# Kernel tuning notes

Hardware: AMD Instinct MI355X
Metric: run time of the kernel (lower is better)

Reference implementation:

```python
import jax, jax.numpy as jnp
import numpy as np

H = 32  # GRU hidden size


def _conv1d(x, w, b, stride, pad):
    # x: (B, Cin, L), w: (Cout, Cin, K)
    y = jax.lax.conv_general_dilated(
        x, w, window_strides=(stride,), padding=[(pad, pad)],
        dimension_numbers=('NCH', 'OIH', 'NCH'))
    return y + b[None, :, None]


def setup_inputs() -> dict:
    key = jax.random.key(0)
    ks = jax.random.split(key, 16)
    B = 16384
    inp = {
        'past_samples': jax.random.normal(ks[0], (B, 2000), jnp.float32),
        'velocity': jax.random.uniform(ks[1], (B,), jnp.float32),
        'log_pitch': jax.random.normal(ks[2], (B,), jnp.float32),
        'time': jax.random.uniform(ks[3], (B,), jnp.float32),
        'hidden_state': jax.random.normal(ks[4], (B, H), jnp.float32),
        # conv stack params
        'w1': jax.random.normal(ks[5], (4, 1, 31), jnp.float32) * 0.1,
        'b1': jnp.zeros((4,), jnp.float32),
        'w2': jax.random.normal(ks[6], (8, 4, 15), jnp.float32) * 0.1,
        'b2': jnp.zeros((8,), jnp.float32),
        'w3': jax.random.normal(ks[7], (16, 8, 7), jnp.float32) * 0.1,
        'b3': jnp.zeros((16,), jnp.float32),
        # GRU params (torch layout: rows = [r; z; n])
        'w_ih': jax.random.normal(ks[8], (3 * H, 19), jnp.float32) * 0.1,
        'w_hh': jax.random.normal(ks[9], (3 * H, H), jnp.float32) * 0.1,
        'b_ih': jnp.zeros((3 * H,), jnp.float32),
        'b_hh': jnp.zeros((3 * H,), jnp.float32),
        # projection
        'w_proj': jax.random.normal(ks[10], (2, H), jnp.float32) * 0.1,
        'b_proj': jnp.zeros((2,), jnp.float32),
    }
    return inp


def reference(past_samples, velocity, log_pitch, time, hidden_state,
              w1, b1, w2, b2, w3, b3, w_ih, w_hh, b_ih, b_hh, w_proj, b_proj):
    x = past_samples[:, None, :]                       # (B,1,2000)
    x = jax.nn.relu(_conv1d(x, w1, b1, 4, 15))         # (B,4,500)
    x = jax.nn.relu(_conv1d(x, w2, b2, 4, 7))          # (B,8,125)
    x = jax.nn.relu(_conv1d(x, w3, b3, 4, 3))          # (B,16,32)
    ctx = jnp.mean(x, axis=2)                          # adaptive avg pool -> (B,16)

    rnn_in = jnp.concatenate(
        [ctx, velocity[:, None], log_pitch[:, None], time[:, None]], axis=1)  # (B,19)

    # single GRU step (torch GRUCell math)
    gi = rnn_in @ w_ih.T + b_ih                        # (B,3H)
    gh = hidden_state @ w_hh.T + b_hh                  # (B,3H)
    r = jax.nn.sigmoid(gi[:, :H] + gh[:, :H])
    z = jax.nn.sigmoid(gi[:, H:2 * H] + gh[:, H:2 * H])
    n = jnp.tanh(gi[:, 2 * H:] + r * gh[:, 2 * H:])
    new_hidden = (1.0 - z) * n + z * hidden_state      # (B,H)

    out = new_hidden @ w_proj.T + b_proj               # (B,2)
    mu, log_sigma = out[:, :1], out[:, 1:]
    sigma = jnp.exp(log_sigma)
    return (mu, sigma, new_hidden)
```

## Files before the change

kernel.cpp:

```cpp
#include <hip/hip_runtime.h>
#include <hip/hip_fp16.h>
#include <math.h>


typedef _Float16 h2 __attribute__((ext_vector_type(2)));
typedef _Float16 h4 __attribute__((ext_vector_type(4)));
typedef _Float16 h8 __attribute__((ext_vector_type(8)));
typedef float f4 __attribute__((ext_vector_type(4)));

__device__ __forceinline__ float fdot2(h2 a, h2 b, float c)
{
#if defined(__has_builtin)
#if __has_builtin(__builtin_amdgcn_fdot2)
    return __builtin_amdgcn_fdot2(a, b, c, false);
#else
    return c + (float)a.x * (float)b.x + (float)a.y * (float)b.y;
#endif
#else
    return c + (float)a.x * (float)b.x + (float)a.y * (float)b.y;
#endif
}

__device__ __forceinline__ h8 ld_b8(const _Float16* p)
{
    h4 lo = *(const h4*)p;
    h4 hi = *(const h4*)(p + 4);
    return (h8){lo.x, lo.y, lo.z, lo.w, hi.x, hi.y, hi.z, hi.w};
}

__global__ void pack_weights(const float* __restrict__ w1,
                             const float* __restrict__ w2,
                             const float* __restrict__ w3,
                             const float* __restrict__ w_ih,
                             _Float16* __restrict__ hws,
                             float* __restrict__ wihp)
{
    for (int idx = threadIdx.x; idx < 64; idx += 256) {
        int c = idx >> 4, jp = idx & 15;
        int j0 = 2 * jp, j1 = j0 + 1;
        float f0 = (j0 == 0) ? 0.0f : w1[c * 31 + j0 - 1];
        float f1 = w1[c * 31 + j1 - 1];
        hws[2 * idx]     = (_Float16)f0;
        hws[2 * idx + 1] = (_Float16)f1;
    }
    for (int i = threadIdx.x; i < 1024; i += 256) {
        int kk = i >> 9, l = (i >> 3) & 63, j = i & 7;
        int c = l & 15, k = kk * 32 + ((l >> 4) << 3) + j;
        int ci = k >> 4, tap = k & 15;
        float v = (c < 8 && tap < 15) ? w2[(c * 4 + ci) * 15 + tap] : 0.0f;
        hws[1024 + i] = (_Float16)v;
    }
    for (int i = threadIdx.x; i < 1024; i += 256) {
        int kk = i >> 9, l = (i >> 3) & 63, j = i & 7;
        int c = l & 15, k = kk * 32 + ((l >> 4) << 3) + j;
        int ci = k >> 3, tap = k & 7;
        float v = (tap < 7) ? w3[(c * 8 + ci) * 7 + tap] : 0.0f;
        hws[2048 + i] = (_Float16)v;
    }
    for (int idx = threadIdx.x; idx < 96 * 20; idx += 256) {
        int r = idx / 20, c = idx % 20;
        wihp[idx] = (c < 19) ? w_ih[r * 19 + c] : 0.0f;
    }
}

__device__ __forceinline__ void conv1_pos(const _Float16* __restrict__ xh,
                                          _Float16* __restrict__ y1h,
                                          const h2* __restrict__ w1p,
                                          const float* __restrict__ b1,
                                          int p, int h0)
{
    const h4* src = (const h4*)(xh + h0);
    h2 xp[16];
#pragma unroll
    for (int j = 0; j < 8; ++j) {
        h4 v = src[j];
        xp[2 * j]     = (h2){v.x, v.y};
        xp[2 * j + 1] = (h2){v.z, v.w};
    }
    float a0 = b1[0], a1 = b1[1], a2 = b1[2], a3 = b1[3];
#pragma unroll
    for (int j = 0; j < 16; ++j) {
        a0 = fdot2(xp[j], w1p[j],      a0);
        a1 = fdot2(xp[j], w1p[16 + j], a1);
        a2 = fdot2(xp[j], w1p[32 + j], a2);
        a3 = fdot2(xp[j], w1p[48 + j], a3);
    }
    y1h[7 + p]        = (_Float16)fmaxf(a0, 0.0f);
    y1h[512 + 7 + p]  = (_Float16)fmaxf(a1, 0.0f);
    y1h[1024 + 7 + p] = (_Float16)fmaxf(a2, 0.0f);
    y1h[1536 + 7 + p] = (_Float16)fmaxf(a3, 0.0f);
}

__global__ void __launch_bounds__(64, 3)
wavernn_fused(const float* __restrict__ past,
              const float* __restrict__ velocity,
              const float* __restrict__ log_pitch,
              const float* __restrict__ time_in,
              const float* __restrict__ hidden,
              const float* __restrict__ b1,
              const float* __restrict__ b2,
              const float* __restrict__ b3,
              const float* __restrict__ wihp,
              const float* __restrict__ w_hh,
              const float* __restrict__ b_ih, const float* __restrict__ b_hh,
              const float* __restrict__ w_proj, const float* __restrict__ b_proj,
              const _Float16* __restrict__ hws,
              float* __restrict__ out, int B)
{
    __shared__ __align__(16) _Float16 X[1056];
    __shared__ __align__(16) _Float16 y1h[2048];
    __shared__ float rnn[20];
    __shared__ float hs[32];

    _Float16* const xbuf = X;
    _Float16* const y2h  = X;
    float* const gis     = (float*)X;
    float* const ghs     = (float*)X + 96;

    const h2* const w1p = (const h2*)hws;
    const h8* const wf2 = (const h8*)(hws + 1024);
    const h8* const wf3 = (const h8*)(hws + 2048);

    const int t = threadIdx.x;
    const int b = blockIdx.x;

    const float4* row4 = (const float4*)(past + (size_t)b * 2000);

    if (t < 16) { xbuf[t] = (_Float16)0.0f; xbuf[1032 + t] = (_Float16)0.0f; }
    if (t < 48) { int c = t / 12, k = t % 12;
                  y1h[c * 512 + (k < 7 ? k : 500 + k)] = (_Float16)0.0f; }
    if (t < 32) hs[t] = hidden[(size_t)b * 32 + t];
    if (t == 0) rnn[16] = velocity[b];
    if (t == 1) rnn[17] = log_pitch[b];
    if (t == 2) rnn[18] = time_in[b];
    if (t == 3) rnn[19] = 0.0f;

#pragma unroll
    for (int j = 0; j < 4; ++j) {
        int i = t + 64 * j;
        if (i < 254) {
            float4 q = row4[i];
            h4 hv = {(_Float16)q.x, (_Float16)q.y, (_Float16)q.z, (_Float16)q.w};
            *(h4*)(xbuf + 16 + 4 * i) = hv;
        }
    }
    __syncthreads();

#pragma unroll
    for (int j = 0; j < 4; ++j) {
        int p = t + 64 * j;
        if (p < 250) conv1_pos(xbuf, y1h, w1p, b1, p, 4 * p);
    }
    __syncthreads();

#pragma unroll
    for (int j = 0; j < 4; ++j) {
        int i = t + 64 * j;
        if (i < 254) {
            float4 q = row4[246 + i];
            h4 hv = {(_Float16)q.x, (_Float16)q.y, (_Float16)q.z, (_Float16)q.w};
            *(h4*)(xbuf + 16 + 4 * i) = hv;
        }
    }
    __syncthreads();

#pragma unroll
    for (int j = 0; j < 4; ++j) {
        int p = 250 + t + 64 * j;
        if (p < 500) conv1_pos(xbuf, y1h, w1p, b1, p, 4 * p - 984);
    }
    __syncthreads();

    if (t < 56) { int c = t / 7, k = t % 7;
                  y2h[c * 132 + (k < 3 ? k : 125 + k)] = (_Float16)0.0f; }
    {
        const int o = t >> 4, q = t & 15;
        const int ci0 = o >> 1, tp0 = (o & 1) * 8;
        float b2v[4];
#pragma unroll
        for (int r = 0; r < 4; ++r) b2v[r] = b2[(o * 4 + r) & 7];
        const h8 a0 = wf2[t];
        const h8 a1 = wf2[64 + t];
#pragma unroll
        for (int T = 0; T < 8; ++T) {
            const int p = T * 16 + q;
            h8 x0 = ld_b8(y1h + 512 * ci0 + 4 * p + tp0);
            h8 x1 = ld_b8(y1h + 512 * (ci0 + 2) + 4 * p + tp0);
            f4 acc = {0.0f, 0.0f, 0.0f, 0.0f};
            acc = __builtin_amdgcn_mfma_f32_16x16x32_f16(a0, x0, acc, 0, 0, 0);
            acc = __builtin_amdgcn_mfma_f32_16x16x32_f16(a1, x1, acc, 0, 0, 0);
            if (t < 32 && p < 125) {
#pragma unroll
                for (int r = 0; r < 4; ++r)
                    y2h[(o * 4 + r) * 132 + 3 + p] =
                        (_Float16)fmaxf(acc[r] + b2v[r], 0.0f);
            }
        }
    }
    __syncthreads();

    {
        const int o = t >> 4, q = t & 15;
        float b3v[4];
#pragma unroll
        for (int r = 0; r < 4; ++r) b3v[r] = b3[o * 4 + r];
        const h8 a0 = wf3[t];
        const h8 a1 = wf3[64 + t];
        h8 x00 = ld_b8(y2h + 132 * o + 4 * q);
        h8 x01 = ld_b8(y2h + 132 * (4 + o) + 4 * q);
        h8 x10 = ld_b8(y2h + 132 * o + 4 * (16 + q));
        h8 x11 = ld_b8(y2h + 132 * (4 + o) + 4 * (16 + q));
        const f4 z = {0.0f, 0.0f, 0.0f, 0.0f};
        f4 d0 = __builtin_amdgcn_mfma_f32_16x16x32_f16(a0, x00, z, 0, 0, 0);
        d0 = __builtin_amdgcn_mfma_f32_16x16x32_f16(a1, x01, d0, 0, 0, 0);
        f4 d1 = __builtin_amdgcn_mfma_f32_16x16x32_f16(a0, x10, z, 0, 0, 0);
        d1 = __builtin_amdgcn_mfma_f32_16x16x32_f16(a1, x11, d1, 0, 0, 0);
#pragma unroll
        for (int r = 0; r < 4; ++r) {
            float v = fmaxf(d0[r] + b3v[r], 0.0f) + fmaxf(d1[r] + b3v[r], 0.0f);
            v += __shfl_xor(v, 1); v += __shfl_xor(v, 2);
            v += __shfl_xor(v, 4); v += __shfl_xor(v, 8);
            if (q == 0) rnn[o * 4 + r] = v * (1.0f / 32.0f);
        }
    }
    __syncthreads();

    {
        float rv[20];
#pragma unroll
        for (int j = 0; j < 20; ++j) rv[j] = rnn[j];

        float a = b_ih[t];
        const float4* wr = (const float4*)(wihp + t * 20);
#pragma unroll
        for (int j = 0; j < 5; ++j) {
            float4 q = wr[j];
            a += rv[4 * j] * q.x + rv[4 * j + 1] * q.y +
                 rv[4 * j + 2] * q.z + rv[4 * j + 3] * q.w;
        }
        gis[t] = a;
        if (t < 32) {
            float a2 = b_ih[64 + t];
            const float4* wr2 = (const float4*)(wihp + (64 + t) * 20);
#pragma unroll
            for (int j = 0; j < 5; ++j) {
                float4 q = wr2[j];
                a2 += rv[4 * j] * q.x + rv[4 * j + 1] * q.y +
                      rv[4 * j + 2] * q.z + rv[4 * j + 3] * q.w;
            }
            gis[64 + t] = a2;
        }

        float hv[32];
#pragma unroll
        for (int j = 0; j < 32; ++j) hv[j] = hs[j];

        float g = b_hh[t];
        const float4* wh = (const float4*)(w_hh + t * 32);
#pragma unroll
        for (int j = 0; j < 8; ++j) {
            float4 q = wh[j];
            g += hv[4 * j] * q.x + hv[4 * j + 1] * q.y +
                 hv[4 * j + 2] * q.z + hv[4 * j + 3] * q.w;
        }
        ghs[t] = g;
        if (t < 32) {
            float g2 = b_hh[64 + t];
            const float4* wh2 = (const float4*)(w_hh + (64 + t) * 32);
#pragma unroll
            for (int j = 0; j < 8; ++j) {
                float4 q = wh2[j];
                g2 += hv[4 * j] * q.x + hv[4 * j + 1] * q.y +
                      hv[4 * j + 2] * q.z + hv[4 * j + 3] * q.w;
            }
            ghs[64 + t] = g2;
        }
    }
    __syncthreads();

    if (t < 32) {
        const int j = t;
        float r = 1.0f / (1.0f + expf(-(gis[j] + ghs[j])));
        float z = 1.0f / (1.0f + expf(-(gis[32 + j] + ghs[32 + j])));
        float n = tanhf(gis[64 + j] + r * ghs[64 + j]);
        float nh = (1.0f - z) * n + z * hs[j];
        out[(size_t)2 * B + (size_t)b * 32 + j] = nh;

        float p0 = nh * w_proj[j];
        float p1 = nh * w_proj[32 + j];
        p0 += __shfl_xor(p0, 16); p1 += __shfl_xor(p1, 16);
        p0 += __shfl_xor(p0, 8);  p1 += __shfl_xor(p1, 8);
        p0 += __shfl_xor(p0, 4);  p1 += __shfl_xor(p1, 4);
        p0 += __shfl_xor(p0, 2);  p1 += __shfl_xor(p1, 2);
        p0 += __shfl_xor(p0, 1);  p1 += __shfl_xor(p1, 1);
        if (j == 0) {
            out[b] = p0 + b_proj[0];
            out[B + b] = expf(p1 + b_proj[1]);
        }
    }
}

extern "C" void kernel_launch(void* const* d_in, const int* in_sizes, int n_in,
                              void* d_out, int out_size, void* d_ws, size_t ws_size,
                              hipStream_t stream)
{
    const float* past      = (const float*)d_in[0];
    const float* velocity  = (const float*)d_in[1];
    const float* log_pitch = (const float*)d_in[2];
    const float* time_in   = (const float*)d_in[3];
    const float* hidden    = (const float*)d_in[4];
    const float* w1  = (const float*)d_in[5];
    const float* b1  = (const float*)d_in[6];
    const float* w2  = (const float*)d_in[7];
    const float* b2  = (const float*)d_in[8];
    const float* w3  = (const float*)d_in[9];
    const float* b3  = (const float*)d_in[10];
    const float* wih = (const float*)d_in[11];
    const float* whh = (const float*)d_in[12];
    const float* bih = (const float*)d_in[13];
    const float* bhh = (const float*)d_in[14];
    const float* wpr = (const float*)d_in[15];
    const float* bpr = (const float*)d_in[16];

    const int B = in_sizes[0] / 2000;
    _Float16* hws = (_Float16*)d_ws;
    float* wihp = (float*)((char*)d_ws + 8192);

    pack_weights<<<dim3(1), dim3(256), 0, stream>>>(w1, w2, w3, wih, hws, wihp);

    wavernn_fused<<<dim3(B), dim3(64), 0, stream>>>(
        past, velocity, log_pitch, time_in, hidden,
        b1, b2, b3, wihp, whh, bih, bhh, wpr, bpr,
        (const _Float16*)hws, (float*)d_out, B);
}
```

Before: 257.1 us.

## Move conv1 to MFMA and switch activations to position-major channel-interleaved layout

Replaces the per-thread fdot2 conv1 with a 16x16x32 MFMA over im2col-style windows and loads the whole 2000-sample row into shared memory at once instead of two halves. Intermediate activations are stored position-major with channels interleaved, so conv2/conv3 operand loads become single aligned h8 reads, and the weight packing is reordered to match. This removes two syncs and the scalar dot-product loop, at the cost of larger shared buffers. Launch bounds also go from 3 to 4 blocks per CU.

```diff
diff --git a/kernel.cpp b/kernel.cpp
--- a/kernel.cpp
+++ b/kernel.cpp
@@ -7,19 +7,6 @@
 typedef _Float16 h4 __attribute__((ext_vector_type(4)));
 typedef _Float16 h8 __attribute__((ext_vector_type(8)));
 typedef float f4 __attribute__((ext_vector_type(4)));
-
-__device__ __forceinline__ float fdot2(h2 a, h2 b, float c)
-{
-#if defined(__has_builtin)
-#if __has_builtin(__builtin_amdgcn_fdot2)
-    return __builtin_amdgcn_fdot2(a, b, c, false);
-#else
-    return c + (float)a.x * (float)b.x + (float)a.y * (float)b.y;
-#endif
-#else
-    return c + (float)a.x * (float)b.x + (float)a.y * (float)b.y;
-#endif
-}
 
 __device__ __forceinline__ h8 ld_b8(const _Float16* p)
 {
@@ -35,27 +22,25 @@
                              _Float16* __restrict__ hws,
                              float* __restrict__ wihp)
 {
-    for (int idx = threadIdx.x; idx < 64; idx += 256) {
-        int c = idx >> 4, jp = idx & 15;
-        int j0 = 2 * jp, j1 = j0 + 1;
-        float f0 = (j0 == 0) ? 0.0f : w1[c * 31 + j0 - 1];
-        float f1 = w1[c * 31 + j1 - 1];
-        hws[2 * idx]     = (_Float16)f0;
-        hws[2 * idx + 1] = (_Float16)f1;
+    for (int i = threadIdx.x; i < 512; i += 256) {
+        int l = i >> 3, j = i & 7;
+        int c = l & 15, k = ((l >> 4) << 3) + j;
+        float v = (c < 4 && k >= 1) ? w1[c * 31 + (k - 1)] : 0.0f;
+        hws[i] = (_Float16)v;
     }
     for (int i = threadIdx.x; i < 1024; i += 256) {
         int kk = i >> 9, l = (i >> 3) & 63, j = i & 7;
         int c = l & 15, k = kk * 32 + ((l >> 4) << 3) + j;
-        int ci = k >> 4, tap = k & 15;
+        int tap = k >> 2, ci = k & 3;
         float v = (c < 8 && tap < 15) ? w2[(c * 4 + ci) * 15 + tap] : 0.0f;
-        hws[1024 + i] = (_Float16)v;
+        hws[512 + i] = (_Float16)v;
     }
     for (int i = threadIdx.x; i < 1024; i += 256) {
         int kk = i >> 9, l = (i >> 3) & 63, j = i & 7;
         int c = l & 15, k = kk * 32 + ((l >> 4) << 3) + j;
-        int ci = k >> 3, tap = k & 7;
+        int tap = k >> 3, ci = k & 7;
         float v = (tap < 7) ? w3[(c * 8 + ci) * 7 + tap] : 0.0f;
-        hws[2048 + i] = (_Float16)v;
+        hws[1536 + i] = (_Float16)v;
     }
     for (int idx = threadIdx.x; idx < 96 * 20; idx += 256) {
         int r = idx / 20, c = idx % 20;
@@ -63,35 +48,7 @@
     }
 }
 
-__device__ __forceinline__ void conv1_pos(const _Float16* __restrict__ xh,
-                                          _Float16* __restrict__ y1h,
-                                          const h2* __restrict__ w1p,
-                                          const float* __restrict__ b1,
-                                          int p, int h0)
-{
-    const h4* src = (const h4*)(xh + h0);
-    h2 xp[16];
-#pragma unroll
-    for (int j = 0; j < 8; ++j) {
-        h4 v = src[j];
-        xp[2 * j]     = (h2){v.x, v.y};
-        xp[2 * j + 1] = (h2){v.z, v.w};
-    }
-    float a0 = b1[0], a1 = b1[1], a2 = b1[2], a3 = b1[3];
-#pragma unroll
-    for (int j = 0; j < 16; ++j) {
-        a0 = fdot2(xp[j], w1p[j],      a0);
-        a1 = fdot2(xp[j], w1p[16 + j], a1);
-        a2 = fdot2(xp[j], w1p[32 + j], a2);
-        a3 = fdot2(xp[j], w1p[48 + j], a3);
-    }
-    y1h[7 + p]        = (_Float16)fmaxf(a0, 0.0f);
-    y1h[512 + 7 + p]  = (_Float16)fmaxf(a1, 0.0f);
-    y1h[1024 + 7 + p] = (_Float16)fmaxf(a2, 0.0f);
-    y1h[1536 + 7 + p] = (_Float16)fmaxf(a3, 0.0f);
-}
-
-__global__ void __launch_bounds__(64, 3)
+__global__ void __launch_bounds__(64, 4)
 wavernn_fused(const float* __restrict__ past,
               const float* __restrict__ velocity,
               const float* __restrict__ log_pitch,
@@ -107,28 +64,31 @@
               const _Float16* __restrict__ hws,
               float* __restrict__ out, int B)
 {
-    __shared__ __align__(16) _Float16 X[1056];
-    __shared__ __align__(16) _Float16 y1h[2048];
+    __shared__ __align__(16) _Float16 X[2080];
+    __shared__ __align__(16) _Float16 y1t[2080];
     __shared__ float rnn[20];
     __shared__ float hs[32];
 
     _Float16* const xbuf = X;
-    _Float16* const y2h  = X;
+    _Float16* const y2t  = X;
     float* const gis     = (float*)X;
     float* const ghs     = (float*)X + 96;
 
-    const h2* const w1p = (const h2*)hws;
-    const h8* const wf2 = (const h8*)(hws + 1024);
-    const h8* const wf3 = (const h8*)(hws + 2048);
+    const h8* const wf1 = (const h8*)hws;
+    const h8* const wf2 = (const h8*)(hws + 512);
+    const h8* const wf3 = (const h8*)(hws + 1536);
 
     const int t = threadIdx.x;
+    const int o = t >> 4;
+    const int q = t & 15;
     const int b = blockIdx.x;
 
     const float4* row4 = (const float4*)(past + (size_t)b * 2000);
 
-    if (t < 16) { xbuf[t] = (_Float16)0.0f; xbuf[1032 + t] = (_Float16)0.0f; }
-    if (t < 48) { int c = t / 12, k = t % 12;
-                  y1h[c * 512 + (k < 7 ? k : 500 + k)] = (_Float16)0.0f; }
+    if (t < 16) xbuf[t] = (_Float16)0.0f;
+    xbuf[2016 + t] = (_Float16)0.0f;
+    if (t < 28) y1t[t] = (_Float16)0.0f;
+    if (t < 52) y1t[2028 + t] = (_Float16)0.0f;
     if (t < 32) hs[t] = hidden[(size_t)b * 32 + t];
     if (t == 0) rnn[16] = velocity[b];
     if (t == 1) rnn[17] = log_pitch[b];
@@ -136,85 +96,78 @@
     if (t == 3) rnn[19] = 0.0f;
 
 #pragma unroll
-    for (int j = 0; j < 4; ++j) {
+    for (int j = 0; j < 8; ++j) {
         int i = t + 64 * j;
-        if (i < 254) {
-            float4 q = row4[i];
-            h4 hv = {(_Float16)q.x, (_Float16)q.y, (_Float16)q.z, (_Float16)q.w};
+        if (i < 500) {
+            float4 v = row4[i];
+            h4 hv = {(_Float16)v.x, (_Float16)v.y, (_Float16)v.z, (_Float16)v.w};
             *(h4*)(xbuf + 16 + 4 * i) = hv;
         }
     }
     __syncthreads();
 
-#pragma unroll
-    for (int j = 0; j < 4; ++j) {
-        int p = t + 64 * j;
-        if (p < 250) conv1_pos(xbuf, y1h, w1p, b1, p, 4 * p);
-    }
-    __syncthreads();
-
-#pragma unroll
-    for (int j = 0; j < 4; ++j) {
-        int i = t + 64 * j;
-        if (i < 254) {
-            float4 q = row4[246 + i];
-            h4 hv = {(_Float16)q.x, (_Float16)q.y, (_Float16)q.z, (_Float16)q.w};
-            *(h4*)(xbuf + 16 + 4 * i) = hv;
-        }
-    }
-    __syncthreads();
-
-#pragma unroll
-    for (int j = 0; j < 4; ++j) {
-        int p = 250 + t + 64 * j;
-        if (p < 500) conv1_pos(xbuf, y1h, w1p, b1, p, 4 * p - 984);
-    }
-    __syncthreads();
-
-    if (t < 56) { int c = t / 7, k = t % 7;
-                  y2h[c * 132 + (k < 3 ? k : 125 + k)] = (_Float16)0.0f; }
-    {
-        const int o = t >> 4, q = t & 15;
-        const int ci0 = o >> 1, tp0 = (o & 1) * 8;
+    {
+        const h8 a1 = wf1[t];
+        const float bv0 = b1[0], bv1 = b1[1], bv2 = b1[2], bv3 = b1[3];
+        const f4 z = {0.0f, 0.0f, 0.0f, 0.0f};
+#pragma unroll
+        for (int T = 0; T < 32; ++T) {
+            const int p = T * 16 + q;
+            h8 x = ld_b8(xbuf + 4 * p + 8 * o);
+            f4 d = __builtin_amdgcn_mfma_f32_16x16x32_f16(a1, x, z, 0, 0, 0);
+            if (o == 0 && p < 500) {
+                h4 w = {(_Float16)fmaxf(d[0] + bv0, 0.0f),
+                        (_Float16)fmaxf(d[1] + bv1, 0.0f),
+                        (_Float16)fmaxf(d[2] + bv2, 0.0f),
+                        (_Float16)fmaxf(d[3] + bv3, 0.0f)};
+                *(h4*)(y1t + (7 + p) * 4) = w;
+            }
+        }
+    }
+    __syncthreads();
+
+    if (t < 24) y2t[t] = (_Float16)0.0f;
+    if (t < 32) y2t[1024 + t] = (_Float16)0.0f;
+    {
+        const h8 a20 = wf2[t];
+        const h8 a21 = wf2[64 + t];
         float b2v[4];
 #pragma unroll
         for (int r = 0; r < 4; ++r) b2v[r] = b2[(o * 4 + r) & 7];
-        const h8 a0 = wf2[t];
-        const h8 a1 = wf2[64 + t];
+        const f4 z = {0.0f, 0.0f, 0.0f, 0.0f};
 #pragma unroll
         for (int T = 0; T < 8; ++T) {
             const int p = T * 16 + q;
-            h8 x0 = ld_b8(y1h + 512 * ci0 + 4 * p + tp0);
-            h8 x1 = ld_b8(y1h + 512 * (ci0 + 2) + 4 * p + tp0);
-            f4 acc = {0.0f, 0.0f, 0.0f, 0.0f};
-            acc = __builtin_amdgcn_mfma_f32_16x16x32_f16(a0, x0, acc, 0, 0, 0);
-            acc = __builtin_amdgcn_mfma_f32_16x16x32_f16(a1, x1, acc, 0, 0, 0);
-            if (t < 32 && p < 125) {
-#pragma unroll
-                for (int r = 0; r < 4; ++r)
-                    y2h[(o * 4 + r) * 132 + 3 + p] =
-                        (_Float16)fmaxf(acc[r] + b2v[r], 0.0f);
-            }
-        }
-    }
-    __syncthreads();
-
-    {
-        const int o = t >> 4, q = t & 15;
+            h8 x0 = *(const h8*)(y1t + 16 * p + 8 * o);
+            h8 x1 = *(const h8*)(y1t + 16 * p + 32 + 8 * o);
+            f4 d = __builtin_amdgcn_mfma_f32_16x16x32_f16(a20, x0, z, 0, 0, 0);
+            d = __builtin_amdgcn_mfma_f32_16x16x32_f16(a21, x1, d, 0, 0, 0);
+            if (o < 2 && p < 125) {
+                h4 w = {(_Float16)fmaxf(d[0] + b2v[0], 0.0f),
+                        (_Float16)fmaxf(d[1] + b2v[1], 0.0f),
+                        (_Float16)fmaxf(d[2] + b2v[2], 0.0f),
+                        (_Float16)fmaxf(d[3] + b2v[3], 0.0f)};
+                *(h4*)(y2t + (3 + p) * 8 + o * 4) = w;
+            }
+        }
+    }
+    __syncthreads();
+
+    {
+        const h8 a30 = wf3[t];
+        const h8 a31 = wf3[64 + t];
         float b3v[4];
 #pragma unroll
         for (int r = 0; r < 4; ++r) b3v[r] = b3[o * 4 + r];
-        const h8 a0 = wf3[t];
-        const h8 a1 = wf3[64 + t];
-        h8 x00 = ld_b8(y2h + 132 * o + 4 * q);
-        h8 x01 = ld_b8(y2h + 132 * (4 + o) + 4 * q);
-        h8 x10 = ld_b8(y2h + 132 * o + 4 * (16 + q));
-        h8 x11 = ld_b8(y2h + 132 * (4 + o) + 4 * (16 + q));
         const f4 z = {0.0f, 0.0f, 0.0f, 0.0f};
-        f4 d0 = __builtin_amdgcn_mfma_f32_16x16x32_f16(a0, x00, z, 0, 0, 0);
-        d0 = __builtin_amdgcn_mfma_f32_16x16x32_f16(a1, x01, d0, 0, 0, 0);
-        f4 d1 = __builtin_amdgcn_mfma_f32_16x16x32_f16(a0, x10, z, 0, 0, 0);
-        d1 = __builtin_amdgcn_mfma_f32_16x16x32_f16(a1, x11, d1, 0, 0, 0);
+        h8 x00 = *(const h8*)(y2t + 32 * q + 8 * o);
+        h8 x01 = *(const h8*)(y2t + 32 * q + 32 + 8 * o);
+        h8 x10 = *(const h8*)(y2t + 32 * (16 + q) + 8 * o);
+        h8 x11 = *(const h8*)(y2t + 32 * (16 + q) + 32 + 8 * o);
+        f4 d0 = __builtin_amdgcn_mfma_f32_16x16x32_f16(a30, x00, z, 0, 0, 0);
+        d0 = __builtin_amdgcn_mfma_f32_16x16x32_f16(a31, x01, d0, 0, 0, 0);
+        f4 d1 = __builtin_amdgcn_mfma_f32_16x16x32_f16(a30, x10, z, 0, 0, 0);
+        d1 = __builtin_amdgcn_mfma_f32_16x16x32_f16(a31, x11, d1, 0, 0, 0);
 #pragma unroll
         for (int r = 0; r < 4; ++r) {
             float v = fmaxf(d0[r] + b3v[r], 0.0f) + fmaxf(d1[r] + b3v[r], 0.0f);
@@ -234,9 +187,9 @@
         const float4* wr = (const float4*)(wihp + t * 20);
 #pragma unroll
         for (int j = 0; j < 5; ++j) {
-            float4 q = wr[j];
-            a += rv[4 * j] * q.x + rv[4 * j + 1] * q.y +
-                 rv[4 * j + 2] * q.z + rv[4 * j + 3] * q.w;
+            float4 qv = wr[j];
+            a += rv[4 * j] * qv.x + rv[4 * j + 1] * qv.y +
+                 rv[4 * j + 2] * qv.z + rv[4 * j + 3] * qv.w;
         }
         gis[t] = a;
         if (t < 32) {
@@ -244,9 +197,9 @@
             const float4* wr2 = (const float4*)(wihp + (64 + t) * 20);
 #pragma unroll
             for (int j = 0; j < 5; ++j) {
-                float4 q = wr2[j];
-                a2 += rv[4 * j] * q.x + rv[4 * j + 1] * q.y +
-                      rv[4 * j + 2] * q.z + rv[4 * j + 3] * q.w;
+                float4 qv = wr2[j];
+                a2 += rv[4 * j] * qv.x + rv[4 * j + 1] * qv.y +
+                      rv[4 * j + 2] * qv.z + rv[4 * j + 3] * qv.w;
             }
             gis[64 + t] = a2;
         }
@@ -259,9 +212,9 @@
         const float4* wh = (const float4*)(w_hh + t * 32);
 #pragma unroll
         for (int j = 0; j < 8; ++j) {
-            float4 q = wh[j];
-            g += hv[4 * j] * q.x + hv[4 * j + 1] * q.y +
-                 hv[4 * j + 2] * q.z + hv[4 * j + 3] * q.w;
+            float4 qv = wh[j];
+            g += hv[4 * j] * qv.x + hv[4 * j + 1] * qv.y +
+                 hv[4 * j + 2] * qv.z + hv[4 * j + 3] * qv.w;
         }
         ghs[t] = g;
         if (t < 32) {
@@ -269,9 +222,9 @@
             const float4* wh2 = (const float4*)(w_hh + (64 + t) * 32);
 #pragma unroll
             for (int j = 0; j < 8; ++j) {
-                float4 q = wh2[j];
-                g2 += hv[4 * j] * q.x + hv[4 * j + 1] * q.y +
-                      hv[4 * j + 2] * q.z + hv[4 * j + 3] * q.w;
+                float4 qv = wh2[j];
+                g2 += hv[4 * j] * qv.x + hv[4 * j + 1] * qv.y +
+                      hv[4 * j + 2] * qv.z + hv[4 * j + 3] * qv.w;
             }
             ghs[64 + t] = g2;
         }
```

New measurement: 266.7 us. 3.8% more time.

## Process two batch rows per 64-thread block to amortize weights and sync

Applied to the files above, without the earlier changes.

Each block now handles two batch samples instead of one, with duplicated shared-memory buffers, and the grid is halved. The weight fragments in registers, the barriers and the per-block launch overhead are shared across both samples, and having two independent streams of loads and MFMAs gives more instruction-level parallelism. In exchange, shared memory per block roughly doubles and register pressure rises; the launch bound is also raised to 4 blocks per CU, which may force register spills.

```diff
diff --git a/kernel.cpp b/kernel.cpp
--- a/kernel.cpp
+++ b/kernel.cpp
@@ -91,7 +91,7 @@
     y1h[1536 + 7 + p] = (_Float16)fmaxf(a3, 0.0f);
 }
 
-__global__ void __launch_bounds__(64, 3)
+__global__ void __launch_bounds__(64, 4)
 wavernn_fused(const float* __restrict__ past,
               const float* __restrict__ velocity,
               const float* __restrict__ log_pitch,
@@ -107,41 +107,46 @@
               const _Float16* __restrict__ hws,
               float* __restrict__ out, int B)
 {
-    __shared__ __align__(16) _Float16 X[1056];
-    __shared__ __align__(16) _Float16 y1h[2048];
-    __shared__ float rnn[20];
-    __shared__ float hs[32];
-
-    _Float16* const xbuf = X;
-    _Float16* const y2h  = X;
-    float* const gis     = (float*)X;
-    float* const ghs     = (float*)X + 96;
+    __shared__ __align__(16) _Float16 X[2][1056];
+    __shared__ __align__(16) _Float16 y1s[2][2048];
+    __shared__ float rnn[2][20];
+    __shared__ float hs[2][32];
 
     const h2* const w1p = (const h2*)hws;
     const h8* const wf2 = (const h8*)(hws + 1024);
     const h8* const wf3 = (const h8*)(hws + 2048);
 
     const int t = threadIdx.x;
-    const int b = blockIdx.x;
-
-    const float4* row4 = (const float4*)(past + (size_t)b * 2000);
-
-    if (t < 16) { xbuf[t] = (_Float16)0.0f; xbuf[1032 + t] = (_Float16)0.0f; }
-    if (t < 48) { int c = t / 12, k = t % 12;
-                  y1h[c * 512 + (k < 7 ? k : 500 + k)] = (_Float16)0.0f; }
-    if (t < 32) hs[t] = hidden[(size_t)b * 32 + t];
-    if (t == 0) rnn[16] = velocity[b];
-    if (t == 1) rnn[17] = log_pitch[b];
-    if (t == 2) rnn[18] = time_in[b];
-    if (t == 3) rnn[19] = 0.0f;
+    const int b0 = blockIdx.x * 2;
+    const bool has2 = (b0 + 1 < B);
+    const int bA = b0, bB = has2 ? b0 + 1 : b0;
+
+    const float4* rowA = (const float4*)(past + (size_t)bA * 2000);
+    const float4* rowB = (const float4*)(past + (size_t)bB * 2000);
+
+#pragma unroll
+    for (int u = 0; u < 2; ++u) {
+        if (t < 16) { X[u][t] = (_Float16)0.0f; X[u][1032 + t] = (_Float16)0.0f; }
+        if (t < 48) { int c = t / 12, k = t % 12;
+                      y1s[u][c * 512 + (k < 7 ? k : 500 + k)] = (_Float16)0.0f; }
+    }
+    if (t < 32) { hs[0][t] = hidden[(size_t)bA * 32 + t];
+                  hs[1][t] = hidden[(size_t)bB * 32 + t]; }
+    if (t == 0) { rnn[0][16] = velocity[bA];  rnn[1][16] = velocity[bB]; }
+    if (t == 1) { rnn[0][17] = log_pitch[bA]; rnn[1][17] = log_pitch[bB]; }
+    if (t == 2) { rnn[0][18] = time_in[bA];   rnn[1][18] = time_in[bB]; }
+    if (t == 3) { rnn[0][19] = 0.0f;          rnn[1][19] = 0.0f; }
 
 #pragma unroll
     for (int j = 0; j < 4; ++j) {
         int i = t + 64 * j;
         if (i < 254) {
-            float4 q = row4[i];
-            h4 hv = {(_Float16)q.x, (_Float16)q.y, (_Float16)q.z, (_Float16)q.w};
-            *(h4*)(xbuf + 16 + 4 * i) = hv;
+            float4 qa = rowA[i];
+            float4 qb = rowB[i];
+            *(h4*)(&X[0][16 + 4 * i]) =
+                (h4){(_Float16)qa.x, (_Float16)qa.y, (_Float16)qa.z, (_Float16)qa.w};
+            *(h4*)(&X[1][16 + 4 * i]) =
+                (h4){(_Float16)qb.x, (_Float16)qb.y, (_Float16)qb.z, (_Float16)qb.w};
         }
     }
     __syncthreads();
@@ -149,7 +154,10 @@
 #pragma unroll
     for (int j = 0; j < 4; ++j) {
         int p = t + 64 * j;
-        if (p < 250) conv1_pos(xbuf, y1h, w1p, b1, p, 4 * p);
+        if (p < 250) {
+            conv1_pos(&X[0][0], &y1s[0][0], w1p, b1, p, 4 * p);
+            conv1_pos(&X[1][0], &y1s[1][0], w1p, b1, p, 4 * p);
+        }
     }
     __syncthreads();
 
@@ -157,9 +165,12 @@
     for (int j = 0; j < 4; ++j) {
         int i = t + 64 * j;
         if (i < 254) {
-            float4 q = row4[246 + i];
-            h4 hv = {(_Float16)q.x, (_Float16)q.y, (_Float16)q.z, (_Float16)q.w};
-            *(h4*)(xbuf + 16 + 4 * i) = hv;
+            float4 qa = rowA[246 + i];
+            float4 qb = rowB[246 + i];
+            *(h4*)(&X[0][16 + 4 * i]) =
+                (h4){(_Float16)qa.x, (_Float16)qa.y, (_Float16)qa.z, (_Float16)qa.w};
+            *(h4*)(&X[1][16 + 4 * i]) =
+                (h4){(_Float16)qb.x, (_Float16)qb.y, (_Float16)qb.z, (_Float16)qb.w};
         }
     }
     __syncthreads();
@@ -167,12 +178,17 @@
 #pragma unroll
     for (int j = 0; j < 4; ++j) {
         int p = 250 + t + 64 * j;
-        if (p < 500) conv1_pos(xbuf, y1h, w1p, b1, p, 4 * p - 984);
-    }
-    __syncthreads();
-
-    if (t < 56) { int c = t / 7, k = t % 7;
-                  y2h[c * 132 + (k < 3 ? k : 125 + k)] = (_Float16)0.0f; }
+        if (p < 500) {
+            conv1_pos(&X[0][0], &y1s[0][0], w1p, b1, p, 4 * p - 984);
+            conv1_pos(&X[1][0], &y1s[1][0], w1p, b1, p, 4 * p - 984);
+        }
+    }
+    __syncthreads();
+
+#pragma unroll
+    for (int u = 0; u < 2; ++u)
+        if (t < 56) { int c = t / 7, k = t % 7;
+                      X[u][c * 132 + (k < 3 ? k : 125 + k)] = (_Float16)0.0f; }
     {
         const int o = t >> 4, q = t & 15;
         const int ci0 = o >> 1, tp0 = (o & 1) * 8;
@@ -181,19 +197,23 @@
         for (int r = 0; r < 4; ++r) b2v[r] = b2[(o * 4 + r) & 7];
         const h8 a0 = wf2[t];
         const h8 a1 = wf2[64 + t];
+        const f4 z = {0.0f, 0.0f, 0.0f, 0.0f};
 #pragma unroll
         for (int T = 0; T < 8; ++T) {
             const int p = T * 16 + q;
-            h8 x0 = ld_b8(y1h + 512 * ci0 + 4 * p + tp0);
-            h8 x1 = ld_b8(y1h + 512 * (ci0 + 2) + 4 * p + tp0);
-            f4 acc = {0.0f, 0.0f, 0.0f, 0.0f};
-            acc = __builtin_amdgcn_mfma_f32_16x16x32_f16(a0, x0, acc, 0, 0, 0);
-            acc = __builtin_amdgcn_mfma_f32_16x16x32_f16(a1, x1, acc, 0, 0, 0);
-            if (t < 32 && p < 125) {
-#pragma unroll
-                for (int r = 0; r < 4; ++r)
-                    y2h[(o * 4 + r) * 132 + 3 + p] =
-                        (_Float16)fmaxf(acc[r] + b2v[r], 0.0f);
+#pragma unroll
+            for (int u = 0; u < 2; ++u) {
+                h8 x0 = ld_b8(&y1s[u][512 * ci0 + 4 * p + tp0]);
+                h8 x1 = ld_b8(&y1s[u][512 * (ci0 + 2) + 4 * p + tp0]);
+                f4 acc = z;
+                acc = __builtin_amdgcn_mfma_f32_16x16x32_f16(a0, x0, acc, 0, 0, 0);
+                acc = __builtin_amdgcn_mfma_f32_16x16x32_f16(a1, x1, acc, 0, 0, 0);
+                if (t < 32 && p < 125) {
+#pragma unroll
+                    for (int r = 0; r < 4; ++r)
+                        X[u][(o * 4 + r) * 132 + 3 + p] =
+                            (_Float16)fmaxf(acc[r] + b2v[r], 0.0f);
+                }
             }
         }
     }
@@ -204,39 +224,47 @@
         float b3v[4];
 #pragma unroll
         for (int r = 0; r < 4; ++r) b3v[r] = b3[o * 4 + r];
-        const h8 a0 = wf3[t];
-        const h8 a1 = wf3[64 + t];
-        h8 x00 = ld_b8(y2h + 132 * o + 4 * q);
-        h8 x01 = ld_b8(y2h + 132 * (4 + o) + 4 * q);
-        h8 x10 = ld_b8(y2h + 132 * o + 4 * (16 + q));
-        h8 x11 = ld_b8(y2h + 132 * (4 + o) + 4 * (16 + q));
+        const h8 a30 = wf3[t];
+        const h8 a31 = wf3[64 + t];
         const f4 z = {0.0f, 0.0f, 0.0f, 0.0f};
-        f4 d0 = __builtin_amdgcn_mfma_f32_16x16x32_f16(a0, x00, z, 0, 0, 0);
-        d0 = __builtin_amdgcn_mfma_f32_16x16x32_f16(a1, x01, d0, 0, 0, 0);
-        f4 d1 = __builtin_amdgcn_mfma_f32_16x16x32_f16(a0, x10, z, 0, 0, 0);
-        d1 = __builtin_amdgcn_mfma_f32_16x16x32_f16(a1, x11, d1, 0, 0, 0);
-#pragma unroll
-        for (int r = 0; r < 4; ++r) {
-            float v = fmaxf(d0[r] + b3v[r], 0.0f) + fmaxf(d1[r] + b3v[r], 0.0f);
-            v += __shfl_xor(v, 1); v += __shfl_xor(v, 2);
-            v += __shfl_xor(v, 4); v += __shfl_xor(v, 8);
-            if (q == 0) rnn[o * 4 + r] = v * (1.0f / 32.0f);
-        }
-    }
-    __syncthreads();
-
-    {
+#pragma unroll
+        for (int u = 0; u < 2; ++u) {
+            const _Float16* y2h = &X[u][0];
+            h8 x00 = ld_b8(y2h + 132 * o + 4 * q);
+            h8 x01 = ld_b8(y2h + 132 * (4 + o) + 4 * q);
+            h8 x10 = ld_b8(y2h + 132 * o + 4 * (16 + q));
+            h8 x11 = ld_b8(y2h + 132 * (4 + o) + 4 * (16 + q));
+            f4 d0 = __builtin_amdgcn_mfma_f32_16x16x32_f16(a30, x00, z, 0, 0, 0);
+            d0 = __builtin_amdgcn_mfma_f32_16x16x32_f16(a31, x01, d0, 0, 0, 0);
+            f4 d1 = __builtin_amdgcn_mfma_f32_16x16x32_f16(a30, x10, z, 0, 0, 0);
+            d1 = __builtin_amdgcn_mfma_f32_16x16x32_f16(a31, x11, d1, 0, 0, 0);
+#pragma unroll
+            for (int r = 0; r < 4; ++r) {
+                float v = fmaxf(d0[r] + b3v[r], 0.0f) + fmaxf(d1[r] + b3v[r], 0.0f);
+                v += __shfl_xor(v, 1); v += __shfl_xor(v, 2);
+                v += __shfl_xor(v, 4); v += __shfl_xor(v, 8);
+                if (q == 0) rnn[u][o * 4 + r] = v * (1.0f / 32.0f);
+            }
+        }
+    }
+    __syncthreads();
+
+#pragma unroll
+    for (int u = 0; u < 2; ++u) {
+        float* const gis = (float*)&X[u][0];
+        float* const ghs = (float*)&X[u][0] + 96;
+
         float rv[20];
 #pragma unroll
-        for (int j = 0; j < 20; ++j) rv[j] = rnn[j];
+        for (int j = 0; j < 20; ++j) rv[j] = rnn[u][j];
 
         float a = b_ih[t];
         const float4* wr = (const float4*)(wihp + t * 20);
 #pragma unroll
         for (int j = 0; j < 5; ++j) {
-            float4 q = wr[j];
-            a += rv[4 * j] * q.x + rv[4 * j + 1] * q.y +
-                 rv[4 * j + 2] * q.z + rv[4 * j + 3] * q.w;
+            float4 qv = wr[j];
+            a += rv[4 * j] * qv.x + rv[4 * j + 1] * qv.y +
+                 rv[4 * j + 2] * qv.z + rv[4 * j + 3] * qv.w;
         }
         gis[t] = a;
         if (t < 32) {
@@ -244,24 +272,24 @@
             const float4* wr2 = (const float4*)(wihp + (64 + t) * 20);
 #pragma unroll
             for (int j = 0; j < 5; ++j) {
-                float4 q = wr2[j];
-                a2 += rv[4 * j] * q.x + rv[4 * j + 1] * q.y +
-                      rv[4 * j + 2] * q.z + rv[4 * j + 3] * q.w;
+                float4 qv = wr2[j];
+                a2 += rv[4 * j] * qv.x + rv[4 * j + 1] * qv.y +
+                      rv[4 * j + 2] * qv.z + rv[4 * j + 3] * qv.w;
             }
             gis[64 + t] = a2;
         }
 
         float hv[32];
 #pragma unroll
-        for (int j = 0; j < 32; ++j) hv[j] = hs[j];
+        for (int j = 0; j < 32; ++j) hv[j] = hs[u][j];
 
         float g = b_hh[t];
         const float4* wh = (const float4*)(w_hh + t * 32);
 #pragma unroll
         for (int j = 0; j < 8; ++j) {
-            float4 q = wh[j];
-            g += hv[4 * j] * q.x + hv[4 * j + 1] * q.y +
-                 hv[4 * j + 2] * q.z + hv[4 * j + 3] * q.w;
+            float4 qv = wh[j];
+            g += hv[4 * j] * qv.x + hv[4 * j + 1] * qv.y +
+                 hv[4 * j + 2] * qv.z + hv[4 * j + 3] * qv.w;
         }
         ghs[t] = g;
         if (t < 32) {
@@ -269,33 +297,40 @@
             const float4* wh2 = (const float4*)(w_hh + (64 + t) * 32);
 #pragma unroll
             for (int j = 0; j < 8; ++j) {
-                float4 q = wh2[j];
-                g2 += hv[4 * j] * q.x + hv[4 * j + 1] * q.y +
-                      hv[4 * j + 2] * q.z + hv[4 * j + 3] * q.w;
+                float4 qv = wh2[j];
+                g2 += hv[4 * j] * qv.x + hv[4 * j + 1] * qv.y +
+                      hv[4 * j + 2] * qv.z + hv[4 * j + 3] * qv.w;
             }
             ghs[64 + t] = g2;
         }
     }
     __syncthreads();
 
-    if (t < 32) {
-        const int j = t;
-        float r = 1.0f / (1.0f + expf(-(gis[j] + ghs[j])));
-        float z = 1.0f / (1.0f + expf(-(gis[32 + j] + ghs[32 + j])));
-        float n = tanhf(gis[64 + j] + r * ghs[64 + j]);
-        float nh = (1.0f - z) * n + z * hs[j];
-        out[(size_t)2 * B + (size_t)b * 32 + j] = nh;
-
-        float p0 = nh * w_proj[j];
-        float p1 = nh * w_proj[32 + j];
-        p0 += __shfl_xor(p0, 16); p1 += __shfl_xor(p1, 16);
-        p0 += __shfl_xor(p0, 8);  p1 += __shfl_xor(p1, 8);
-        p0 += __shfl_xor(p0, 4);  p1 += __shfl_xor(p1, 4);
-        p0 += __shfl_xor(p0, 2);  p1 += __shfl_xor(p1, 2);
-        p0 += __shfl_xor(p0, 1);  p1 += __shfl_xor(p1, 1);
-        if (j == 0) {
-            out[b] = p0 + b_proj[0];
-            out[B + b] = expf(p1 + b_proj[1]);
+#pragma unroll
+    for (int u = 0; u < 2; ++u) {
+        if (u == 1 && !has2) break;
+        const int bb = u ? bB : bA;
+        float* const gis = (float*)&X[u][0];
+        float* const ghs = (float*)&X[u][0] + 96;
+        if (t < 32) {
+            const int j = t;
+            float r = 1.0f / (1.0f + expf(-(gis[j] + ghs[j])));
+            float z = 1.0f / (1.0f + expf(-(gis[32 + j] + ghs[32 + j])));
+            float n = tanhf(gis[64 + j] + r * ghs[64 + j]);
+            float nh = (1.0f - z) * n + z * hs[u][j];
+            out[(size_t)2 * B + (size_t)bb * 32 + j] = nh;
+
+            float p0 = nh * w_proj[j];
+            float p1 = nh * w_proj[32 + j];
+            p0 += __shfl_xor(p0, 16); p1 += __shfl_xor(p1, 16);
+            p0 += __shfl_xor(p0, 8);  p1 += __shfl_xor(p1, 8);
+            p0 += __shfl_xor(p0, 4);  p1 += __shfl_xor(p1, 4);
+            p0 += __shfl_xor(p0, 2);  p1 += __shfl_xor(p1, 2);
+            p0 += __shfl_xor(p0, 1);  p1 += __shfl_xor(p1, 1);
+            if (j == 0) {
+                out[bb] = p0 + b_proj[0];
+                out[B + bb] = expf(p1 + b_proj[1]);
+            }
         }
     }
 }
@@ -328,7 +363,8 @@
 
     pack_weights<<<dim3(1), dim3(256), 0, stream>>>(w1, w2, w3, wih, hws, wihp);
 
-    wavernn_fused<<<dim3(B), dim3(64), 0, stream>>>(
+    const int nblk = (B + 1) / 2;
+    wavernn_fused<<<dim3(nblk), dim3(64), 0, stream>>>(
         past, velocity, log_pitch, time_in, hidden,
         b1, b2, b3, wihp, whh, bih, bhh, wpr, bpr,
         (const _Float16*)hws, (float*)d_out, B);
```

New measurement: 262.5 us. 2.1% more time.
